# Performance work log

Hardware: AMD Instinct MI355X
Metric: run time of the kernel (lower is better)

## Reference

```python
import math
import jax, jax.numpy as jnp
import numpy as np

B, N, M, C, H = 64, 64, 64, 512, 8
HD = C // H
FREQ = 256  # frequency_embedding_size
MAX_PERIOD = 10000.0


def setup_inputs() -> dict:
    key = jax.random.key(0)
    ks = jax.random.split(key, 10)
    s = 1.0 / math.sqrt(C)
    sf = 1.0 / math.sqrt(FREQ)
    return {
        "query": jax.random.normal(ks[0], (B, N, C), jnp.float32),
        "query_pos": jax.random.uniform(ks[1], (1, N, M), jnp.float32),
        # projection weights stored as [in, out]
        "Wq": jax.random.normal(ks[2], (C, C), jnp.float32) * s,
        "bq": jnp.zeros((C,), jnp.float32),
        "Wk": jax.random.normal(ks[3], (C, C), jnp.float32) * s,  # no bias
        "Wv": jax.random.normal(ks[4], (C, C), jnp.float32) * s,
        "bv": jnp.zeros((C,), jnp.float32),
        "Wo": jax.random.normal(ks[5], (C, C), jnp.float32) * s,
        "bo": jnp.zeros((C,), jnp.float32),
        # ScalarEmbedder MLP: Linear(FREQ->C), SiLU, Linear(C->C)
        "W1": jax.random.normal(ks[6], (FREQ, C), jnp.float32) * sf,
        "b1": jnp.zeros((C,), jnp.float32),
        "W2": jax.random.normal(ks[7], (C, C), jnp.float32) * s,
        "b2": jnp.zeros((C,), jnp.float32),
    }


def _freqs():
    half = FREQ // 2
    return jnp.exp(-math.log(MAX_PERIOD) * jnp.arange(half, dtype=jnp.float32) / half)


def reference(query, query_pos, Wq, bq, Wk, Wv, bv, Wo, bo, W1, b1, W2, b2):
    Bq, Nq, Cq = query.shape
    Mk = query_pos.shape[-1]
    # --- ScalarEmbedder on flattened pairwise positions: [N*M] -> [N*M, C]
    t = query_pos.reshape(-1)                       # [Bp*N*M], Bp = 1
    tf = t[:, None] * _freqs()[None, :]             # [N*M, FREQ/2]
    emb = jnp.concatenate([jnp.cos(tf), jnp.sin(tf)], axis=-1)  # [N*M, FREQ]
    pe = jax.nn.silu(emb @ W1 + b1) @ W2 + b2        # [N*M, C]
    pe = pe.reshape(Nq, Mk, H, HD).transpose(2, 0, 1, 3)  # [H, N, M, hd] (tiled over B via broadcast)

    q = (query @ Wq + bq).reshape(Bq, Nq, H, HD)     # bnhd
    k = (query @ Wk).reshape(Bq, Mk, H, HD)          # bmhd (key = query)
    v = (query @ Wv + bv).reshape(Bq, Mk, H, HD)

    scale = HD ** -0.5
    # attn[b,h,n,m] = sum_d q[b,n,h,d] * pe[h,n,m,d] * k[b,m,h,d]
    scores = jnp.einsum("bnhd,hnmd,bmhd->bhnm", q, pe, k) * scale
    attn = jax.nn.softmax(scores, axis=-1)
    x = jnp.einsum("bhnm,bmhd->bnhd", attn, v).reshape(Bq, Nq, Cq)
    return x @ Wo + bo + query  # identity = query
```

## Files before the change

### kernel.cpp

```cpp
#include <hip/hip_runtime.h>
#include <hip/hip_bf16.h>
#include <math.h>

typedef short short8 __attribute__((ext_vector_type(8)));
typedef float floatx4 __attribute__((ext_vector_type(4)));

__device__ __forceinline__ ushort f2bf(float f) {
    __hip_bfloat16 h = __float2bfloat16(f);
    return *reinterpret_cast<ushort*>(&h);
}
__device__ __forceinline__ void bf8_to_f32(uint4 u, float* f) {
    f[0] = __uint_as_float(u.x << 16); f[1] = __uint_as_float(u.x & 0xffff0000u);
    f[2] = __uint_as_float(u.y << 16); f[3] = __uint_as_float(u.y & 0xffff0000u);
    f[4] = __uint_as_float(u.z << 16); f[5] = __uint_as_float(u.z & 0xffff0000u);
    f[6] = __uint_as_float(u.w << 16); f[7] = __uint_as_float(u.w & 0xffff0000u);
}

#define GLDS16(g, l) __builtin_amdgcn_global_load_lds( \
    (const __attribute__((address_space(1))) void*)(g), \
    (__attribute__((address_space(3))) void*)(l), 16, 0, 0)

__global__ __launch_bounds__(256) void prep_kernel(
        const float* __restrict__ W1, const float* __restrict__ W2,
        const float* __restrict__ Wq, const float* __restrict__ Wk,
        const float* __restrict__ Wv, const float* __restrict__ Wo,
        const float* __restrict__ bq, const float* __restrict__ bv,
        const float* __restrict__ query, const float* __restrict__ qpos,
        ushort* __restrict__ W1t, ushort* __restrict__ W2t,
        ushort* __restrict__ Wqkvt, ushort* __restrict__ Wot,
        ushort* __restrict__ queryB, ushort* __restrict__ embB,
        float* __restrict__ biasC) {
    const int z = blockIdx.z;
    const int tx = threadIdx.x, ty = threadIdx.y;
    const int tid = ty * 32 + tx;
    if (z < 6) {
        const float* src; ushort* dst; int R;
        switch (z) {
            case 0:  src = W1; dst = W1t;              R = 256; break;
            case 1:  src = W2; dst = W2t;              R = 512; break;
            case 2:  src = Wq; dst = Wqkvt;            R = 512; break;
            case 3:  src = Wk; dst = Wqkvt + 512*512;  R = 512; break;
            case 4:  src = Wv; dst = Wqkvt + 1024*512; R = 512; break;
            default: src = Wo; dst = Wot;              R = 512; break;
        }
        const int r0 = blockIdx.y * 32, c0 = blockIdx.x * 32;
        if (r0 >= R) return;
        __shared__ float t[32][33];
        for (int i = ty; i < 32; i += 8) t[i][tx] = src[(size_t)(r0 + i) * 512 + c0 + tx];
        __syncthreads();
        for (int i = ty; i < 32; i += 8) dst[(size_t)(c0 + i) * R + r0 + tx] = f2bf(t[tx][i]);
    } else if (z == 6) {
        const int bid = blockIdx.y * 16 + blockIdx.x;
#pragma unroll
        for (int i = 0; i < 8; ++i) {
            size_t idx4 = (size_t)bid * 2048 + i * 256 + tid;
            float4 v = *(const float4*)(query + idx4 * 4);
            ushort4 o; o.x = f2bf(v.x); o.y = f2bf(v.y); o.z = f2bf(v.z); o.w = f2bf(v.w);
            *(ushort4*)(queryB + idx4 * 4) = o;
        }
        if (bid == 0) {
            for (int i = tid; i < 1536; i += 256)
                biasC[i] = (i < 512) ? bq[i] : ((i < 1024) ? 0.0f : bv[i - 1024]);
        }
    } else {
        const int bid = blockIdx.y * 16 + blockIdx.x;
        const int gt = bid * 256 + tid;
        const int e0 = gt * 16;
        const int r = e0 >> 8, j0 = e0 & 255;
        const float t = qpos[r];
        ushort o[16];
#pragma unroll
        for (int u = 0; u < 16; ++u) {
            int j = j0 + u, i = j & 127;
            float freq = __expf(-9.210340371976184f * (float)i * (1.0f / 128.0f));
            float a = t * freq;
            o[u] = f2bf((j < 128) ? __cosf(a) : __sinf(a));
        }
        *(uint4*)(embB + e0)     = *(uint4*)&o[0];
        *(uint4*)(embB + e0 + 8) = *(uint4*)&o[8];
    }
}

__global__ __launch_bounds__(256) void gemm_bf16(
        const ushort* __restrict__ A, const ushort* __restrict__ Bt,
        const float* __restrict__ bias, const float* __restrict__ resid,
        void* __restrict__ Cout, int M, int N, int K, int act, int out_fp32) {
    __shared__ ushort As[64 * 32];
    __shared__ ushort Bs[64 * 32];
    const int tid = threadIdx.x;
    const int l = tid & 63, w = tid >> 6;
    const int wr = w >> 1, wc = w & 1;
    const int row0 = blockIdx.x * 64, col0 = blockIdx.y * 64;
    const int l15 = l & 15, quad = l >> 4;
    const int arow = w * 16 + (l >> 2), koff = (l & 3) * 8;

    const ushort* gA = A  + (size_t)(row0 + arow) * K + koff;
    const ushort* gB = Bt + (size_t)(col0 + arow) * K + koff;
    ushort* lA = &As[w * 512 + l * 8];
    ushort* lB = &Bs[w * 512 + l * 8];

    floatx4 acc[2][2] = {};

    for (int k0 = 0; k0 < K; k0 += 32) {
        __syncthreads();
        GLDS16(gA + k0, lA);
        GLDS16(gB + k0, lB);
        __syncthreads();
        short8 a0 = *(const short8*)&As[(wr * 32 + l15) * 32 + quad * 8];
        short8 a1 = *(const short8*)&As[(wr * 32 + 16 + l15) * 32 + quad * 8];
        short8 b0 = *(const short8*)&Bs[(wc * 32 + l15) * 32 + quad * 8];
        short8 b1 = *(const short8*)&Bs[(wc * 32 + 16 + l15) * 32 + quad * 8];
        acc[0][0] = __builtin_amdgcn_mfma_f32_16x16x32_bf16(a0, b0, acc[0][0], 0, 0, 0);
        acc[0][1] = __builtin_amdgcn_mfma_f32_16x16x32_bf16(a0, b1, acc[0][1], 0, 0, 0);
        acc[1][0] = __builtin_amdgcn_mfma_f32_16x16x32_bf16(a1, b0, acc[1][0], 0, 0, 0);
        acc[1][1] = __builtin_amdgcn_mfma_f32_16x16x32_bf16(a1, b1, acc[1][1], 0, 0, 0);
    }

#pragma unroll
    for (int i = 0; i < 2; ++i)
#pragma unroll
        for (int j = 0; j < 2; ++j) {
            int col = col0 + wc * 32 + j * 16 + l15;
            float bvv = bias ? bias[col] : 0.0f;
#pragma unroll
            for (int r = 0; r < 4; ++r) {
                int row = row0 + wr * 32 + i * 16 + quad * 4 + r;
                float val = acc[i][j][r] + bvv;
                if (act) val = val / (1.0f + __expf(-val));
                if (out_fp32) {
                    float rv = resid ? resid[(size_t)row * N + col] : 0.0f;
                    ((float*)Cout)[(size_t)row * N + col] = val + rv;
                } else {
                    ((ushort*)Cout)[(size_t)row * N + col] = f2bf(val);
                }
            }
        }
}

__global__ __launch_bounds__(256) void attn_bf16(
        const ushort* __restrict__ qkv, const ushort* __restrict__ peB,
        ushort* __restrict__ xB) {
    const int h = blockIdx.x, b = blockIdx.y, nh = blockIdx.z;
    const int tid = threadIdx.x;
    const int w = tid >> 6, l = tid & 63;
    const int lo = l & 7, hi = l >> 3;

    __shared__ float ks[64 * 64];
    __shared__ float vs[64 * 64];
    __shared__ float qs[32 * 64];

#pragma unroll
    for (int p = 0; p < 2; ++p) {
        int cid = p * 256 + tid;
        int row = cid >> 3, ch = cid & 7;
        const ushort* base = qkv + (size_t)(b * 64 + row) * 1536 + h * 64 + ch * 8;
        uint4 ku = *(const uint4*)(base + 512);
        uint4 vu = *(const uint4*)(base + 1024);
        float kf[8], vf[8];
        bf8_to_f32(ku, kf); bf8_to_f32(vu, vf);
#pragma unroll
        for (int j = 0; j < 8; ++j) {
            ks[row * 64 + ch * 8 + j] = kf[j];
            vs[row * 64 + ch * 8 + j] = vf[j];
        }
    }
    {
        int row = tid >> 3, ch = tid & 7;
        uint4 qu = *(const uint4*)(qkv + (size_t)(b * 64 + nh * 32 + row) * 1536 + h * 64 + ch * 8);
        float qf[8]; bf8_to_f32(qu, qf);
#pragma unroll
        for (int j = 0; j < 8; ++j) qs[row * 64 + ch * 8 + j] = qf[j];
    }
    __syncthreads();

    for (int i = 0; i < 8; ++i) {
        int nl = w + 4 * i;
        int n = nh * 32 + nl;
        float qf[8];
        *(float4*)&qf[0] = *(const float4*)&qs[nl * 64 + lo * 8];
        *(float4*)&qf[4] = *(const float4*)&qs[nl * 64 + lo * 8 + 4];

        float sreg[8];
#pragma unroll
        for (int mg = 0; mg < 8; ++mg) {
            int m = mg * 8 + hi;
            uint4 pu = *(const uint4*)(peB + (size_t)(n * 64 + m) * 512 + h * 64 + lo * 8);
            float pf[8]; bf8_to_f32(pu, pf);
            float kf[8];
            *(float4*)&kf[0] = *(const float4*)&ks[m * 64 + lo * 8];
            *(float4*)&kf[4] = *(const float4*)&ks[m * 64 + lo * 8 + 4];
            float p = 0.0f;
#pragma unroll
            for (int j = 0; j < 8; ++j) p = fmaf(qf[j] * kf[j], pf[j], p);
            p += __shfl_xor(p, 1);
            p += __shfl_xor(p, 2);
            p += __shfl_xor(p, 4);
            sreg[mg] = p * 0.125f;
        }

        float mx = sreg[0];
#pragma unroll
        for (int mg = 1; mg < 8; ++mg) mx = fmaxf(mx, sreg[mg]);
        mx = fmaxf(mx, __shfl_xor(mx, 8));
        mx = fmaxf(mx, __shfl_xor(mx, 16));
        mx = fmaxf(mx, __shfl_xor(mx, 32));
        float sum = 0.0f;
#pragma unroll
        for (int mg = 0; mg < 8; ++mg) { sreg[mg] = __expf(sreg[mg] - mx); sum += sreg[mg]; }
        sum += __shfl_xor(sum, 8);
        sum += __shfl_xor(sum, 16);
        sum += __shfl_xor(sum, 32);
        float rs = 1.0f / sum;

        float acc[8] = {};
#pragma unroll
        for (int mg = 0; mg < 8; ++mg) {
            int m = mg * 8 + hi;
            float at = sreg[mg] * rs;
            float vf[8];
            *(float4*)&vf[0] = *(const float4*)&vs[m * 64 + lo * 8];
            *(float4*)&vf[4] = *(const float4*)&vs[m * 64 + lo * 8 + 4];
#pragma unroll
            for (int j = 0; j < 8; ++j) acc[j] = fmaf(at, vf[j], acc[j]);
        }
#pragma unroll
        for (int j = 0; j < 8; ++j) {
            acc[j] += __shfl_xor(acc[j], 8);
            acc[j] += __shfl_xor(acc[j], 16);
            acc[j] += __shfl_xor(acc[j], 32);
        }
        if (l < 8) {
            uint4 o;
            o.x = f2bf(acc[0]) | ((uint)f2bf(acc[1]) << 16);
            o.y = f2bf(acc[2]) | ((uint)f2bf(acc[3]) << 16);
            o.z = f2bf(acc[4]) | ((uint)f2bf(acc[5]) << 16);
            o.w = f2bf(acc[6]) | ((uint)f2bf(acc[7]) << 16);
            *(uint4*)(xB + (size_t)(b * 64 + n) * 512 + h * 64 + l * 8) = o;
        }
    }
}

extern "C" void kernel_launch(void* const* d_in, const int* in_sizes, int n_in,
                              void* d_out, int out_size, void* d_ws, size_t ws_size,
                              hipStream_t stream) {
    const float* query = (const float*)d_in[0];
    const float* qpos  = (const float*)d_in[1];
    const float* Wq    = (const float*)d_in[2];
    const float* bq    = (const float*)d_in[3];
    const float* Wk    = (const float*)d_in[4];
    const float* Wv    = (const float*)d_in[5];
    const float* bv    = (const float*)d_in[6];
    const float* Wo    = (const float*)d_in[7];
    const float* bo    = (const float*)d_in[8];
    const float* W1    = (const float*)d_in[9];
    const float* b1    = (const float*)d_in[10];
    const float* W2    = (const float*)d_in[11];
    const float* b2    = (const float*)d_in[12];
    float* out = (float*)d_out;
    char* ws = (char*)d_ws;

    ushort* W1t    = (ushort*)(ws + 0);
    ushort* W2t    = (ushort*)(ws + 262144);
    ushort* Wqkvt  = (ushort*)(ws + 786432);
    ushort* Wot    = (ushort*)(ws + 2359296);
    float*  biasC  = (float*) (ws + 2883584);
    ushort* embB   = (ushort*)(ws + 3145728);
    ushort* queryB = (ushort*)(ws + 5242880);
    ushort* hiddenB= (ushort*)(ws + 9437184);
    ushort* peB    = (ushort*)(ws + 13631488);
    ushort* qkvB   = (ushort*)(ws + 17825792);
    ushort* xB     = (ushort*)(ws + 30408704);

    prep_kernel<<<dim3(16, 16, 8), dim3(32, 8), 0, stream>>>(
        W1, W2, Wq, Wk, Wv, Wo, bq, bv, query, qpos,
        W1t, W2t, Wqkvt, Wot, queryB, embB, biasC);

    gemm_bf16<<<dim3(64, 8),  256, 0, stream>>>(embB,    W1t,   b1,    nullptr, hiddenB, 4096,  512, 256, 1, 0);
    gemm_bf16<<<dim3(64, 8),  256, 0, stream>>>(hiddenB, W2t,   b2,    nullptr, peB,     4096,  512, 512, 0, 0);
    gemm_bf16<<<dim3(64, 24), 256, 0, stream>>>(queryB,  Wqkvt, biasC, nullptr, qkvB,    4096, 1536, 512, 0, 0);

    attn_bf16<<<dim3(8, 64, 2), 256, 0, stream>>>(qkvB, peB, xB);

    gemm_bf16<<<dim3(64, 8),  256, 0, stream>>>(xB, Wot, bo, query, out, 4096, 512, 512, 0, 1);
}
```

Measured before the change: 163.7 us.

## Fuse positional-embedding MLP into one kernel and restructure attention to bf16 LDS

Merges the sinusoidal embedding generation, the W1+SiLU GEMM and the W2 GEMM into a single kernel. Each block handles 16 rows and keeps the embedding and hidden activations in shared memory, which removes two launches and the global round-trips for emb and hidden. The attention kernel now stores K/V as bf16 in LDS (halving LDS use), reads q directly from global, and uses a 64x8x4 grid with 16 query rows per block for more parallelism. The cost is that the fused kernel streams W1t/W2t from global without LDS tiling, across only 256 blocks.

```diff
diff --git a/kernel.cpp b/kernel.cpp
--- a/kernel.cpp
+++ b/kernel.cpp
@@ -25,11 +25,10 @@
         const float* __restrict__ Wq, const float* __restrict__ Wk,
         const float* __restrict__ Wv, const float* __restrict__ Wo,
         const float* __restrict__ bq, const float* __restrict__ bv,
-        const float* __restrict__ query, const float* __restrict__ qpos,
+        const float* __restrict__ query,
         ushort* __restrict__ W1t, ushort* __restrict__ W2t,
         ushort* __restrict__ Wqkvt, ushort* __restrict__ Wot,
-        ushort* __restrict__ queryB, ushort* __restrict__ embB,
-        float* __restrict__ biasC) {
+        ushort* __restrict__ queryB, float* __restrict__ biasC) {
     const int z = blockIdx.z;
     const int tx = threadIdx.x, ty = threadIdx.y;
     const int tid = ty * 32 + tx;
@@ -49,7 +48,7 @@
         for (int i = ty; i < 32; i += 8) t[i][tx] = src[(size_t)(r0 + i) * 512 + c0 + tx];
         __syncthreads();
         for (int i = ty; i < 32; i += 8) dst[(size_t)(c0 + i) * R + r0 + tx] = f2bf(t[tx][i]);
-    } else if (z == 6) {
+    } else {
         const int bid = blockIdx.y * 16 + blockIdx.x;
 #pragma unroll
         for (int i = 0; i < 8; ++i) {
@@ -62,22 +61,80 @@
             for (int i = tid; i < 1536; i += 256)
                 biasC[i] = (i < 512) ? bq[i] : ((i < 1024) ? 0.0f : bv[i - 1024]);
         }
-    } else {
-        const int bid = blockIdx.y * 16 + blockIdx.x;
-        const int gt = bid * 256 + tid;
-        const int e0 = gt * 16;
-        const int r = e0 >> 8, j0 = e0 & 255;
-        const float t = qpos[r];
-        ushort o[16];
-#pragma unroll
-        for (int u = 0; u < 16; ++u) {
+    }
+}
+
+__global__ __launch_bounds__(512) void pe_fused(
+        const float* __restrict__ qpos,
+        const ushort* __restrict__ W1t, const ushort* __restrict__ W2t,
+        const float* __restrict__ b1, const float* __restrict__ b2,
+        ushort* __restrict__ peB) {
+    __shared__ ushort embS[16 * 256];
+    __shared__ ushort hidS[16 * 512];
+    const int tid = threadIdx.x;
+    const int l = tid & 63, w = tid >> 6;
+    const int l15 = l & 15, quad = l >> 4;
+    const int r0 = blockIdx.x * 16;
+
+    {
+        const int e0 = tid * 8;
+        const int row = e0 >> 8, j0 = e0 & 255;
+        const float t = qpos[r0 + row];
+        ushort o[8];
+#pragma unroll
+        for (int u = 0; u < 8; ++u) {
             int j = j0 + u, i = j & 127;
             float freq = __expf(-9.210340371976184f * (float)i * (1.0f / 128.0f));
             float a = t * freq;
             o[u] = f2bf((j < 128) ? __cosf(a) : __sinf(a));
         }
-        *(uint4*)(embB + e0)     = *(uint4*)&o[0];
-        *(uint4*)(embB + e0 + 8) = *(uint4*)&o[8];
+        *(uint4*)&embS[e0] = *(uint4*)&o[0];
+    }
+    __syncthreads();
+
+    {
+        floatx4 acc[4] = {};
+        for (int k0 = 0; k0 < 256; k0 += 32) {
+            short8 a = *(const short8*)&embS[l15 * 256 + k0 + quad * 8];
+#pragma unroll
+            for (int j = 0; j < 4; ++j) {
+                short8 bf = *(const short8*)(W1t + (size_t)(w * 64 + j * 16 + l15) * 256 + k0 + quad * 8);
+                acc[j] = __builtin_amdgcn_mfma_f32_16x16x32_bf16(a, bf, acc[j], 0, 0, 0);
+            }
+        }
+#pragma unroll
+        for (int j = 0; j < 4; ++j) {
+            int col = w * 64 + j * 16 + l15;
+            float bb = b1[col];
+#pragma unroll
+            for (int r = 0; r < 4; ++r) {
+                int row = quad * 4 + r;
+                float v = acc[j][r] + bb;
+                v = v / (1.0f + __expf(-v));
+                hidS[row * 512 + col] = f2bf(v);
+            }
+        }
+    }
+    __syncthreads();
+
+    {
+        floatx4 acc[4] = {};
+        for (int k0 = 0; k0 < 512; k0 += 32) {
+            short8 a = *(const short8*)&hidS[l15 * 512 + k0 + quad * 8];
+#pragma unroll
+            for (int j = 0; j < 4; ++j) {
+                short8 bf = *(const short8*)(W2t + (size_t)(w * 64 + j * 16 + l15) * 512 + k0 + quad * 8);
+                acc[j] = __builtin_amdgcn_mfma_f32_16x16x32_bf16(a, bf, acc[j], 0, 0, 0);
+            }
+        }
+#pragma unroll
+        for (int j = 0; j < 4; ++j) {
+            int col = w * 64 + j * 16 + l15;
+            float bb = b2[col];
+#pragma unroll
+            for (int r = 0; r < 4; ++r)
+                peB[(size_t)(r0 + quad * 4 + r) * 512 + col] = f2bf(acc[j][r] + bb);
+        }
     }
 }
 
@@ -137,48 +194,34 @@
         }
 }
 
-__global__ __launch_bounds__(256) void attn_bf16(
+__global__ __launch_bounds__(256) void attn_hi(
         const ushort* __restrict__ qkv, const ushort* __restrict__ peB,
         ushort* __restrict__ xB) {
-    const int h = blockIdx.x, b = blockIdx.y, nh = blockIdx.z;
+    const int b = blockIdx.x, h = blockIdx.y, ng = blockIdx.z;
     const int tid = threadIdx.x;
     const int w = tid >> 6, l = tid & 63;
     const int lo = l & 7, hi = l >> 3;
 
-    __shared__ float ks[64 * 64];
-    __shared__ float vs[64 * 64];
-    __shared__ float qs[32 * 64];
-
-#pragma unroll
-    for (int p = 0; p < 2; ++p) {
-        int cid = p * 256 + tid;
-        int row = cid >> 3, ch = cid & 7;
-        const ushort* base = qkv + (size_t)(b * 64 + row) * 1536 + h * 64 + ch * 8;
-        uint4 ku = *(const uint4*)(base + 512);
-        uint4 vu = *(const uint4*)(base + 1024);
-        float kf[8], vf[8];
-        bf8_to_f32(ku, kf); bf8_to_f32(vu, vf);
-#pragma unroll
-        for (int j = 0; j < 8; ++j) {
-            ks[row * 64 + ch * 8 + j] = kf[j];
-            vs[row * 64 + ch * 8 + j] = vf[j];
-        }
-    }
-    {
-        int row = tid >> 3, ch = tid & 7;
-        uint4 qu = *(const uint4*)(qkv + (size_t)(b * 64 + nh * 32 + row) * 1536 + h * 64 + ch * 8);
+    __shared__ ushort ksB[64 * 64];
+    __shared__ ushort vsB[64 * 64];
+
+#pragma unroll
+    for (int p = 0; p < 4; ++p) {
+        int idx = p * 256 + tid;
+        int mat = idx >> 9, c = idx & 511;
+        int row = c >> 3, ch = c & 7;
+        const ushort* src = qkv + (size_t)(b * 64 + row) * 1536
+                          + (mat ? 1024 : 512) + h * 64 + ch * 8;
+        uint4 u = *(const uint4*)src;
+        ushort* dst = (mat ? vsB : ksB) + row * 64 + ch * 8;
+        *(uint4*)dst = u;
+    }
+    __syncthreads();
+
+    for (int i = 0; i < 4; ++i) {
+        const int n = ng * 16 + w + 4 * i;
+        uint4 qu = *(const uint4*)(qkv + (size_t)(b * 64 + n) * 1536 + h * 64 + lo * 8);
         float qf[8]; bf8_to_f32(qu, qf);
-#pragma unroll
-        for (int j = 0; j < 8; ++j) qs[row * 64 + ch * 8 + j] = qf[j];
-    }
-    __syncthreads();
-
-    for (int i = 0; i < 8; ++i) {
-        int nl = w + 4 * i;
-        int n = nh * 32 + nl;
-        float qf[8];
-        *(float4*)&qf[0] = *(const float4*)&qs[nl * 64 + lo * 8];
-        *(float4*)&qf[4] = *(const float4*)&qs[nl * 64 + lo * 8 + 4];
 
         float sreg[8];
 #pragma unroll
@@ -186,9 +229,8 @@
             int m = mg * 8 + hi;
             uint4 pu = *(const uint4*)(peB + (size_t)(n * 64 + m) * 512 + h * 64 + lo * 8);
             float pf[8]; bf8_to_f32(pu, pf);
-            float kf[8];
-            *(float4*)&kf[0] = *(const float4*)&ks[m * 64 + lo * 8];
-            *(float4*)&kf[4] = *(const float4*)&ks[m * 64 + lo * 8 + 4];
+            uint4 ku = *(const uint4*)&ksB[m * 64 + lo * 8];
+            float kf[8]; bf8_to_f32(ku, kf);
             float p = 0.0f;
 #pragma unroll
             for (int j = 0; j < 8; ++j) p = fmaf(qf[j] * kf[j], pf[j], p);
@@ -217,9 +259,8 @@
         for (int mg = 0; mg < 8; ++mg) {
             int m = mg * 8 + hi;
             float at = sreg[mg] * rs;
-            float vf[8];
-            *(float4*)&vf[0] = *(const float4*)&vs[m * 64 + lo * 8];
-            *(float4*)&vf[4] = *(const float4*)&vs[m * 64 + lo * 8 + 4];
+            uint4 vu = *(const uint4*)&vsB[m * 64 + lo * 8];
+            float vf[8]; bf8_to_f32(vu, vf);
 #pragma unroll
             for (int j = 0; j < 8; ++j) acc[j] = fmaf(at, vf[j], acc[j]);
         }
@@ -264,22 +305,22 @@
     ushort* Wqkvt  = (ushort*)(ws + 786432);
     ushort* Wot    = (ushort*)(ws + 2359296);
     float*  biasC  = (float*) (ws + 2883584);
-    ushort* embB   = (ushort*)(ws + 3145728);
     ushort* queryB = (ushort*)(ws + 5242880);
-    ushort* hiddenB= (ushort*)(ws + 9437184);
     ushort* peB    = (ushort*)(ws + 13631488);
     ushort* qkvB   = (ushort*)(ws + 17825792);
     ushort* xB     = (ushort*)(ws + 30408704);
 
-    prep_kernel<<<dim3(16, 16, 8), dim3(32, 8), 0, stream>>>(
-        W1, W2, Wq, Wk, Wv, Wo, bq, bv, query, qpos,
-        W1t, W2t, Wqkvt, Wot, queryB, embB, biasC);
-
-    gemm_bf16<<<dim3(64, 8),  256, 0, stream>>>(embB,    W1t,   b1,    nullptr, hiddenB, 4096,  512, 256, 1, 0);
-    gemm_bf16<<<dim3(64, 8),  256, 0, stream>>>(hiddenB, W2t,   b2,    nullptr, peB,     4096,  512, 512, 0, 0);
-    gemm_bf16<<<dim3(64, 24), 256, 0, stream>>>(queryB,  Wqkvt, biasC, nullptr, qkvB,    4096, 1536, 512, 0, 0);
-
-    attn_bf16<<<dim3(8, 64, 2), 256, 0, stream>>>(qkvB, peB, xB);
-
-    gemm_bf16<<<dim3(64, 8),  256, 0, stream>>>(xB, Wot, bo, query, out, 4096, 512, 512, 0, 1);
-}
+    prep_kernel<<<dim3(16, 16, 7), dim3(32, 8), 0, stream>>>(
+        W1, W2, Wq, Wk, Wv, Wo, bq, bv, query,
+        W1t, W2t, Wqkvt, Wot, queryB, biasC);
+
+    pe_fused<<<256, 512, 0, stream>>>(qpos, W1t, W2t, b1, b2, peB);
+
+    gemm_bf16<<<dim3(64, 24), 256, 0, stream>>>(queryB, Wqkvt, biasC, nullptr,
+                                                qkvB, 4096, 1536, 512, 0, 0);
+
+    attn_hi<<<dim3(64, 8, 4), 256, 0, stream>>>(qkvB, peB, xB);
+
+    gemm_bf16<<<dim3(64, 8), 256, 0, stream>>>(xB, Wot, bo, query, out,
+                                               4096, 512, 512, 0, 1);
+}
```

Measured after the change: 176.0 us. +7.5%, slower.
